# Optimization experiments

Measured on AMD Instinct MI355X. Metric: run time of the kernel, lower is better.

The kernel has to match this reference:

```python
import jax, jax.numpy as jnp
import numpy as np

NT, NGRID, NX = 512, 2048, 16   # time steps, grids/basins, total input features
NY, HID, D = 1, 64, 4           # outputs, hidden size, max delay (lag window)


def setup_inputs() -> dict:
    key = jax.random.key(0)
    ks = jax.random.split(key, 8)
    s_in = 1.0 / np.sqrt(NX).astype(np.float32)
    s_h = 1.0 / np.sqrt(HID).astype(np.float32)
    u = lambda k, shape, s: jax.random.uniform(k, shape, jnp.float32, -s, s)
    return {
        "x": jax.random.normal(ks[0], (NT, NGRID, NX), jnp.float32),
        "W_in": u(ks[1], (NX, HID), s_in),
        "b_in": u(ks[2], (HID,), s_in),
        "W_xh": u(ks[3], (HID, HID), s_h),
        "W_hh": u(ks[4], (HID, HID), s_h),
        "b_h": u(ks[5], (HID,), s_h),
        "W_out": u(ks[6], (HID, NY), s_h),
        "b_out": u(ks[7], (NY,), s_h),
    }


def reference(x, W_in, b_in, W_xh, W_hh, b_h, W_out, b_out):
    nt, ngrid, nx = x.shape
    T = nt - D  # number of predicted steps (t = D .. nt-1)
    # lag-window gather: for output t, window covers x[t-D : t]
    idx = jnp.arange(T)[:, None] + jnp.arange(D)[None, :]  # [T, D]
    exog = x[..., : nx - NY][idx]   # [T, D, ngrid, nx-ny] exogenous inputs
    feed = x[..., nx - NY:][idx]    # [T, D, ngrid, ny]    feedback (observed y)
    win = jnp.concatenate([exog, feed], axis=-1)  # [T, D, ngrid, nx]
    win = jnp.moveaxis(win, 1, 0)                 # [D, T, ngrid, nx] scan over delay

    def step(h, x_d):
        u = jax.nn.relu(x_d @ W_in + b_in)           # linearIn + ReLU
        h_new = jnp.tanh(u @ W_xh + h @ W_hh + b_h)  # Narx (tanh RNN) cell
        return h_new, None

    h0 = jnp.zeros((T, ngrid, HID), x.dtype)
    hT, _ = jax.lax.scan(step, h0, win)   # final hidden state over the window
    yt = hT @ W_out + b_out               # [T, ngrid, ny] linearOut
    out = jnp.zeros((nt, ngrid, NY), x.dtype).at[D:].set(yt)
    return out
```

## Files before the change

### kernel.cpp

```cpp
#include <hip/hip_runtime.h>
#include <hip/hip_bf16.h>


#define NG    2048
#define NXF   16
#define HIDN  64
#define DLAG  4
#define TOUTN 508
#define GBLK  64
#define TTB   4
#define NSLC  (DLAG + TTB - 1)
#define STR   72
#define SW    40
#define SCALE 2.8853900817779268f

typedef short  s16x8 __attribute__((ext_vector_type(8)));
typedef float  f32x4 __attribute__((ext_vector_type(4)));
typedef unsigned int u32x4 __attribute__((ext_vector_type(4)));

__device__ __forceinline__ unsigned short f2bf(float f) {
    unsigned int u = __float_as_uint(f);
    u += 0x7fffu + ((u >> 16) & 1u);
    return (unsigned short)(u >> 16);
}
__device__ __forceinline__ unsigned int pk2bf(float a, float b) {
    union { __hip_bfloat162 h2; unsigned int u; } c;
    c.h2 = __float22bfloat162_rn(float2{a, b});
    return c.u;
}
__device__ __forceinline__ float tanh_pre(float a) {
    float e = exp2f(a);
    return fmaf(-2.0f, __builtin_amdgcn_rcpf(e + 1.0f), 1.0f);
}

__global__ __launch_bounds__(256, 3)
void narx_kernel(const float* __restrict__ x,
                 const float* __restrict__ Win,
                 const float* __restrict__ bin_g,
                 const float* __restrict__ Wxh,
                 const float* __restrict__ Whh,
                 const float* __restrict__ bh_g,
                 const float* __restrict__ Wout,
                 const float* __restrict__ bout_g,
                 float* __restrict__ out)
{
    __shared__ unsigned short s_stage[HIDN * STR];
    __shared__ unsigned short s_win[HIDN * SW];

    const int tid   = threadIdx.x;
    const int lane  = tid & 63;
    const int lm    = lane & 15;
    const int q     = lane >> 4;
    const int G0    = blockIdx.x * GBLK;
    const int tt0   = blockIdx.y * TTB;
    const int wrow0 = (tid >> 6) * 16;
    const int myg   = G0 + wrow0 + lm;

    if (blockIdx.y == 0 && tid < GBLK) {
        #pragma unroll
        for (int t2 = 0; t2 < DLAG; ++t2)
            out[t2 * NG + G0 + tid] = 0.0f;
    }

    {
        int r = tid >> 2, c0 = 16 + (tid & 3) * 4;
        #pragma unroll
        for (int i = 0; i < 4; ++i) {
            unsigned short v = 0;
            if (c0 + i == 16) v = f2bf(bin_g[r]);
            s_win[r * SW + c0 + i] = v;
        }
    }

    const int p0  = tid >> 2;
    const int pi0 = 32*(p0>>5) + 16*((p0>>2)&1) + 4*((p0>>3)&3) + (p0&3);
    const int n0  = (tid & 3) * 16;

    s16x8 wxhf[4][2], whhf[4][2];
    {
        const float* src = Wxh + pi0 * HIDN + n0;
        #pragma unroll
        for (int i = 0; i < 16; ++i)
            s_stage[(n0 + i) * STR + p0] = f2bf(src[i] * SCALE);
    }
    __syncthreads();
    #pragma unroll
    for (int tn = 0; tn < 4; ++tn)
        #pragma unroll
        for (int kk = 0; kk < 2; ++kk)
            wxhf[tn][kk] = *(const s16x8*)&s_stage[(tn*16 + lm) * STR + kk*32 + q*8];
    __syncthreads();
    {
        const float* src = Whh + pi0 * HIDN + n0;
        #pragma unroll
        for (int i = 0; i < 16; ++i)
            s_stage[(n0 + i) * STR + p0] = f2bf(src[i] * SCALE);
    }
    __syncthreads();
    #pragma unroll
    for (int tn = 0; tn < 4; ++tn)
        #pragma unroll
        for (int kk = 0; kk < 2; ++kk)
            whhf[tn][kk] = *(const s16x8*)&s_stage[(tn*16 + lm) * STR + kk*32 + q*8];

    {
        int k = tid >> 4, nn = (tid & 15) * 4;
        const float* src = Win + k * HIDN + nn;
        #pragma unroll
        for (int i = 0; i < 4; ++i) s_win[(nn + i) * SW + k] = f2bf(src[i]);
    }

    f32x4 bhf4[4];
    #pragma unroll
    for (int tn = 0; tn < 4; ++tn) {
        f32x4 h4 = *(const f32x4*)&bh_g[tn*16 + q*4];
        bhf4[tn] = h4 * SCALE;
    }
    const float boutf = bout_g[0];
    __syncthreads();

    const size_t slcstride = (size_t)NG * NXF;
    const float* px = x + ((size_t)tt0 * NG + myg) * NXF + q * 8;

    auto load_pack = [&](int s) -> s16x8 {
        s16x8 r = {0,0,0,0,0,0,0,0};
        if (q == 2) r[0] = (short)0x3F80;
        if (q < 2) {
            const float* p = px + (size_t)s * slcstride;
            f32x4 a = *(const f32x4*)p;
            f32x4 b = *(const f32x4*)(p + 4);
            u32x4 xi;
            xi[0] = pk2bf(a[0], a[1]);
            xi[1] = pk2bf(a[2], a[3]);
            xi[2] = pk2bf(b[0], b[1]);
            xi[3] = pk2bf(b[2], b[3]);
            r = __builtin_bit_cast(s16x8, xi);
        }
        return r;
    };

    u32x4 hpk[TTB][2];
    s16x8 xf = load_pack(0);

    #pragma unroll
    for (int s = 0; s < NSLC; ++s) {
        s16x8 xf_nxt = xf;
        if (s + 1 < NSLC) xf_nxt = load_pack(s + 1);

        u32x4 upk[2];
        #pragma unroll
        for (int tj = 0; tj < 4; ++tj) {
            s16x8 wf = *(const s16x8*)&s_win[(tj*16 + lm) * SW + q*8];
            f32x4 zc = {0.f, 0.f, 0.f, 0.f};
            f32x4 ua = __builtin_amdgcn_mfma_f32_16x16x32_bf16(wf, xf, zc, 0, 0, 0);
            upk[tj>>1][(tj&1)*2+0] = pk2bf(fmaxf(ua[0],0.f), fmaxf(ua[1],0.f));
            upk[tj>>1][(tj&1)*2+1] = pk2bf(fmaxf(ua[2],0.f), fmaxf(ua[3],0.f));
        }
        const s16x8 uf0 = __builtin_bit_cast(s16x8, upk[0]);
        const s16x8 uf1 = __builtin_bit_cast(s16x8, upk[1]);

        #pragma unroll
        for (int ti = 0; ti < TTB; ++ti) {
            if (ti > s || ti < s - (DLAG - 1)) continue;

            f32x4 ha[4];
            #pragma unroll
            for (int tn = 0; tn < 4; ++tn)
                ha[tn] = __builtin_amdgcn_mfma_f32_16x16x32_bf16(
                    wxhf[tn][0], uf0, bhf4[tn], 0, 0, 0);
            #pragma unroll
            for (int tn = 0; tn < 4; ++tn)
                ha[tn] = __builtin_amdgcn_mfma_f32_16x16x32_bf16(
                    wxhf[tn][1], uf1, ha[tn], 0, 0, 0);

            if (ti != s) {
                #pragma unroll
                for (int kk = 0; kk < 2; ++kk) {
                    s16x8 hf = __builtin_bit_cast(s16x8, hpk[ti][kk]);
                    #pragma unroll
                    for (int tn = 0; tn < 4; ++tn)
                        ha[tn] = __builtin_amdgcn_mfma_f32_16x16x32_bf16(
                            whhf[tn][kk], hf, ha[tn], 0, 0, 0);
                }
            }

            if (ti > s - (DLAG - 1)) {
                #pragma unroll
                for (int tn = 0; tn < 4; ++tn) {
                    hpk[ti][tn>>1][(tn&1)*2+0] =
                        pk2bf(tanh_pre(ha[tn][0]), tanh_pre(ha[tn][1]));
                    hpk[ti][tn>>1][(tn&1)*2+1] =
                        pk2bf(tanh_pre(ha[tn][2]), tanh_pre(ha[tn][3]));
                }
            } else {
                float acc = 0.f;
                #pragma unroll
                for (int tn = 0; tn < 4; ++tn) {
                    f32x4 wo = *(const f32x4*)&Wout[tn*16 + q*4];
                    #pragma unroll
                    for (int r = 0; r < 4; ++r)
                        acc += tanh_pre(ha[tn][r]) * wo[r];
                }
                acc += __shfl_xor(acc, 16, 64);
                acc += __shfl_xor(acc, 32, 64);
                if (lane < 16)
                    out[(size_t)(tt0 + ti + DLAG) * NG + G0 + wrow0 + lane] =
                        acc + boutf;
            }
        }

        xf = xf_nxt;
    }
}

extern "C" void kernel_launch(void* const* d_in, const int* in_sizes, int n_in,
                              void* d_out, int out_size, void* d_ws, size_t ws_size,
                              hipStream_t stream) {
    const float* x    = (const float*)d_in[0];
    const float* Win  = (const float*)d_in[1];
    const float* bin  = (const float*)d_in[2];
    const float* Wxh  = (const float*)d_in[3];
    const float* Whh  = (const float*)d_in[4];
    const float* bh   = (const float*)d_in[5];
    const float* Wout = (const float*)d_in[6];
    const float* bout = (const float*)d_in[7];
    float* out = (float*)d_out;

    dim3 grid(NG / GBLK, TOUTN / TTB);
    narx_kernel<<<grid, dim3(256), 0, stream>>>(x, Win, bin, Wxh, Whh, bh, Wout, bout, out);
}
```

Measured before the change: 217.0 us.

## Prepack recurrent weights into MFMA fragments in a separate pre-kernel

```diff
diff --git a/kernel.cpp b/kernel.cpp
--- a/kernel.cpp
+++ b/kernel.cpp
@@ -13,6 +13,8 @@
 #define STR   72
 #define SW    40
 #define SCALE 2.8853900817779268f
+#define WXH_OFF 0
+#define WHH_OFF 4096
 
 typedef short  s16x8 __attribute__((ext_vector_type(8)));
 typedef float  f32x4 __attribute__((ext_vector_type(4)));
@@ -28,23 +30,77 @@
     c.h2 = __float22bfloat162_rn(float2{a, b});
     return c.u;
 }
+__device__ __forceinline__ float raw_exp2(float a) {
+#if __has_builtin(__builtin_amdgcn_exp2f)
+    return __builtin_amdgcn_exp2f(a);
+#else
+    float r;
+    asm("v_exp_f32 %0, %1" : "=v"(r) : "v"(a));
+    return r;
+#endif
+}
 __device__ __forceinline__ float tanh_pre(float a) {
-    float e = exp2f(a);
+    float e = raw_exp2(a);
     return fmaf(-2.0f, __builtin_amdgcn_rcpf(e + 1.0f), 1.0f);
+}
+
+__global__ __launch_bounds__(256, 1)
+void pack_weights(const float* __restrict__ Wxh,
+                  const float* __restrict__ Whh,
+                  unsigned short* __restrict__ ws)
+{
+    __shared__ unsigned short s_stage[HIDN * STR];
+    const int tid  = threadIdx.x;
+    const int lane = tid & 63;
+    const int lm   = lane & 15;
+    const int q    = lane >> 4;
+    const int p0   = tid >> 2;
+    const int pi0  = 32*(p0>>5) + 16*((p0>>2)&1) + 4*((p0>>3)&3) + (p0&3);
+    const int n0   = (tid & 3) * 16;
+
+    {
+        const float* src = Wxh + pi0 * HIDN + n0;
+        #pragma unroll
+        for (int i = 0; i < 16; ++i)
+            s_stage[(n0 + i) * STR + p0] = f2bf(src[i] * SCALE);
+    }
+    __syncthreads();
+    if (tid < 64) {
+        #pragma unroll
+        for (int tn = 0; tn < 4; ++tn)
+            #pragma unroll
+            for (int kk = 0; kk < 2; ++kk)
+                *(s16x8*)&ws[WXH_OFF + lane*64 + tn*16 + kk*8] =
+                    *(const s16x8*)&s_stage[(tn*16 + lm) * STR + kk*32 + q*8];
+    }
+    __syncthreads();
+    {
+        const float* src = Whh + pi0 * HIDN + n0;
+        #pragma unroll
+        for (int i = 0; i < 16; ++i)
+            s_stage[(n0 + i) * STR + p0] = f2bf(src[i] * SCALE);
+    }
+    __syncthreads();
+    if (tid < 64) {
+        #pragma unroll
+        for (int tn = 0; tn < 4; ++tn)
+            #pragma unroll
+            for (int kk = 0; kk < 2; ++kk)
+                *(s16x8*)&ws[WHH_OFF + lane*64 + tn*16 + kk*8] =
+                    *(const s16x8*)&s_stage[(tn*16 + lm) * STR + kk*32 + q*8];
+    }
 }
 
 __global__ __launch_bounds__(256, 3)
 void narx_kernel(const float* __restrict__ x,
                  const float* __restrict__ Win,
                  const float* __restrict__ bin_g,
-                 const float* __restrict__ Wxh,
-                 const float* __restrict__ Whh,
+                 const unsigned short* __restrict__ wfrag,
                  const float* __restrict__ bh_g,
                  const float* __restrict__ Wout,
                  const float* __restrict__ bout_g,
                  float* __restrict__ out)
 {
-    __shared__ unsigned short s_stage[HIDN * STR];
     __shared__ unsigned short s_win[HIDN * SW];
 
     const int tid   = threadIdx.x;
@@ -62,6 +118,15 @@
             out[t2 * NG + G0 + tid] = 0.0f;
     }
 
+    s16x8 wxhf[4][2], whhf[4][2];
+    #pragma unroll
+    for (int tn = 0; tn < 4; ++tn)
+        #pragma unroll
+        for (int kk = 0; kk < 2; ++kk) {
+            wxhf[tn][kk] = *(const s16x8*)&wfrag[WXH_OFF + lane*64 + tn*16 + kk*8];
+            whhf[tn][kk] = *(const s16x8*)&wfrag[WHH_OFF + lane*64 + tn*16 + kk*8];
+        }
+
     {
         int r = tid >> 2, c0 = 16 + (tid & 3) * 4;
         #pragma unroll
@@ -71,38 +136,6 @@
             s_win[r * SW + c0 + i] = v;
         }
     }
-
-    const int p0  = tid >> 2;
-    const int pi0 = 32*(p0>>5) + 16*((p0>>2)&1) + 4*((p0>>3)&3) + (p0&3);
-    const int n0  = (tid & 3) * 16;
-
-    s16x8 wxhf[4][2], whhf[4][2];
-    {
-        const float* src = Wxh + pi0 * HIDN + n0;
-        #pragma unroll
-        for (int i = 0; i < 16; ++i)
-            s_stage[(n0 + i) * STR + p0] = f2bf(src[i] * SCALE);
-    }
-    __syncthreads();
-    #pragma unroll
-    for (int tn = 0; tn < 4; ++tn)
-        #pragma unroll
-        for (int kk = 0; kk < 2; ++kk)
-            wxhf[tn][kk] = *(const s16x8*)&s_stage[(tn*16 + lm) * STR + kk*32 + q*8];
-    __syncthreads();
-    {
-        const float* src = Whh + pi0 * HIDN + n0;
-        #pragma unroll
-        for (int i = 0; i < 16; ++i)
-            s_stage[(n0 + i) * STR + p0] = f2bf(src[i] * SCALE);
-    }
-    __syncthreads();
-    #pragma unroll
-    for (int tn = 0; tn < 4; ++tn)
-        #pragma unroll
-        for (int kk = 0; kk < 2; ++kk)
-            whhf[tn][kk] = *(const s16x8*)&s_stage[(tn*16 + lm) * STR + kk*32 + q*8];
-
     {
         int k = tid >> 4, nn = (tid & 15) * 4;
         const float* src = Win + k * HIDN + nn;
@@ -225,7 +258,10 @@
     const float* Wout = (const float*)d_in[6];
     const float* bout = (const float*)d_in[7];
     float* out = (float*)d_out;
+    unsigned short* ws = (unsigned short*)d_ws;
+
+    pack_weights<<<dim3(1), dim3(256), 0, stream>>>(Wxh, Whh, ws);
 
     dim3 grid(NG / GBLK, TOUTN / TTB);
-    narx_kernel<<<grid, dim3(256), 0, stream>>>(x, Win, bin, Wxh, Whh, bh, Wout, bout, out);
-}
+    narx_kernel<<<grid, dim3(256), 0, stream>>>(x, Win, bin, ws, bh, Wout, bout, out);
+}
```

Result: faster. 205.7 us (-5.2%).
